# Kernel tuning notes

Hardware: AMD Instinct MI355X
Metric: run time of the kernel (lower is better)

## Reference

```python
import jax, jax.numpy as jnp
import numpy as np

P = 384   # ssm_size
H = 768   # hidden_dim
K = 4     # conv_kernel
BATCH, LEN = 16, 2048


def setup_inputs() -> dict:
    key = jax.random.key(0)
    ks = jax.random.split(key, 12)
    inputs = jax.random.normal(ks[0], (BATCH, LEN, H), jnp.float32)
    # encoder
    Wl = jax.random.normal(ks[1], (H, H), jnp.float32) / np.sqrt(H)
    bl = jnp.zeros((H,), jnp.float32)
    conv_w = jax.random.normal(ks[2], (H, 1, K), jnp.float32) / np.sqrt(K)  # depthwise
    conv_b = jnp.zeros((H,), jnp.float32)
    # selective heads (zero-init in torch; small random for a non-trivial baseline)
    Wr = jax.random.normal(ks[3], (P, H), jnp.float32) * 0.01
    Wth = jax.random.normal(ks[4], (P, H), jnp.float32) * 0.01
    Winj = jax.random.normal(ks[5], (P, H), jnp.float32) * 0.01
    # ring init: |lambda| in [0.9, 1.0], arg in (0, pi)
    u = jax.random.uniform(ks[6], (P,), jnp.float32)
    mags = jnp.sqrt(u * (1.0 ** 2 - 0.9 ** 2) + 0.9 ** 2)
    r_base = jnp.log(mags / (1.0 - mags))              # logit
    args = jax.random.uniform(ks[7], (P,), jnp.float32, minval=1e-3, maxval=np.pi - 1e-3)
    th_base = jnp.arctanh(args / np.pi)
    dt_base = jax.random.normal(ks[8], (P,), jnp.float32) * 0.5
    inj_logit = jnp.full((P,), 2.0, jnp.float32)
    b_std = 1.0 / np.sqrt(H)
    c_std = 1.0 / np.sqrt(P)
    Bp = jax.random.uniform(ks[9], (P, H, 2), jnp.float32, minval=-b_std, maxval=b_std)
    Cp = jax.random.uniform(ks[10], (H, P, 2), jnp.float32, minval=-c_std, maxval=c_std)
    D = jax.random.normal(ks[11], (H,), jnp.float32)
    return dict(inputs=inputs, Wl=Wl, bl=bl, conv_w=conv_w, conv_b=conv_b,
                Wr=Wr, Wth=Wth, Winj=Winj, r_base=r_base, th_base=th_base,
                dt_base=dt_base, inj_logit=inj_logit, Bp=Bp, Cp=Cp, D=D)


def reference(inputs, Wl, bl, conv_w, conv_b, Wr, Wth, Winj,
              r_base, th_base, dt_base, inj_logit, Bp, Cp, D):
    Bsz, L, Hd = inputs.shape
    k = conv_w.shape[-1]
    # --- encoder: linear -> silu -> causal depthwise conv -> silu ---
    feats = jax.nn.silu(inputs @ Wl.T + bl)                       # (B,L,H)
    fc = jnp.transpose(feats, (0, 2, 1))                          # (B,H,L)
    fc = jax.lax.conv_general_dilated(
        fc, conv_w, window_strides=(1,), padding=[(k - 1, 0)],
        dimension_numbers=('NCH', 'OIH', 'NCH'), feature_group_count=Hd)
    feats = jnp.transpose(jax.nn.silu(fc + conv_b[None, :, None]), (0, 2, 1))  # (B,L,H)
    # --- spectral params ---
    r = jax.nn.sigmoid(r_base + feats @ Wr.T)                     # (B,L,P)
    theta = jnp.pi * jnp.tanh(th_base + feats @ Wth.T)            # (B,L,P)
    dt_floor = 0.02
    raw_dt = jax.nn.sigmoid(dt_base)                              # (P,) per_step_dt=False
    dt = jnp.broadcast_to(dt_floor + (1.0 - dt_floor) * raw_dt, r.shape)
    r2 = jnp.maximum(r * r, 1e-8)
    dtc = jnp.maximum(dt, 1e-6)
    cos_t = jnp.cos(theta)
    # imex1 variant
    A = (r2 - 2.0 * r * cos_t + 1.0) / (dtc * dtc * r2)
    G = (1.0 - r2) / (dtc * r2)
    # --- input projection (complex) + selective injection gate ---
    Bc = Bp[..., 0] + 1j * Bp[..., 1]                             # (P,H) complex64
    Cc = Cp[..., 0] + 1j * Cp[..., 1]                             # (H,P)
    bu = inputs.astype(jnp.complex64) @ Bc.T                      # (B,L,P)
    gate = jax.nn.sigmoid(inj_logit + feats @ Winj.T)
    bu = bu * gate
    # --- D-LinOSS IMEX1 scan over time ---
    A_s = jnp.transpose(A, (1, 0, 2))                             # (L,B,P)
    G_s = jnp.transpose(G, (1, 0, 2))
    dt_s = jnp.transpose(dtc, (1, 0, 2))
    bu_s = jnp.transpose(bu, (1, 0, 2))
    z0 = jnp.zeros((Bsz, A.shape[-1]), jnp.complex64)

    def step(carry, t):
        z, x = carry
        At, Gt, dtt, but = t
        S = 1.0 / (1.0 + dtt * Gt)          # implicit damping factor
        z = S * (z - (dtt * At) * x) + (S * dtt) * but
        x = x + dtt * z
        return (z, x), x

    _, xs = jax.lax.scan(step, (z0, z0), (A_s, G_s, dt_s, bu_s))  # (L,B,P)
    states = jnp.transpose(xs, (1, 0, 2))                         # (B,L,P)
    proj = jnp.real(states @ Cc.T)                                # (B,L,H)
    return proj + inputs * D
```

## Files before the change

kernel.cpp:

```cpp
#include <hip/hip_runtime.h>
#include <math.h>

#define PP 384
#define HH 768
#define KK 4
#define BB 16
#define LL 2048
#define MM (BB*LL)
#define NCH (BB*PP)
#define NC 32
#define CLEN (LL/NC)
#define CRUN 32

typedef __attribute__((ext_vector_type(8))) short bf16x8;
typedef __attribute__((ext_vector_type(4))) float f32x4;

__device__ __forceinline__ float sigmoid_fast(float x) { return 1.0f / (1.0f + __expf(-x)); }

__device__ __forceinline__ float bf2f(unsigned short h) {
    return __uint_as_float(((unsigned int)h) << 16);
}
__device__ __forceinline__ unsigned short f2bf(float x) {
    unsigned int u = __float_as_uint(x);
    u += 0x7fff + ((u >> 16) & 1);
    return (unsigned short)(u >> 16);
}
__device__ __forceinline__ void split_bf(float x, unsigned short& hi, unsigned short& lo) {
    hi = f2bf(x);
    lo = f2bf(x - bf2f(hi));
}

__device__ __forceinline__ void gll16(const void* g, void* l) {
    __builtin_amdgcn_global_load_lds(
        (const __attribute__((address_space(1))) void*)g,
        (__attribute__((address_space(3))) void*)l, 16, 0, 0);
}

__device__ __forceinline__ void xcd_swizzle(int& bx, int& by) {
    const int gx = (int)gridDim.x;
    const int nwg = gx * (int)gridDim.y;
    const int orig = by * gx + bx;
    const int q = nwg >> 3, r = nwg & 7;
    const int xcd = orig & 7, off = orig >> 3;
    const int swz = (xcd < r ? xcd * (q + 1) : r * (q + 1) + (xcd - r) * q) + off;
    bx = swz % gx;
    by = swz / gx;
}

__device__ __forceinline__ void step_coef(float Rp, float Tp, float Ip,
    float rb, float tb, float il, float dt,
    float& c0, float& c1, float& gdt)
{
    const float PIf = 3.14159265358979323846f;
    float r  = sigmoid_fast(rb + Rp);
    float t  = tb + Tp;
    float e2 = __expf(2.0f * fabsf(t));
    float th = PIf * copysignf(1.0f - 2.0f / (e2 + 1.0f), t);
    float ct = __cosf(th);
    float r2 = fmaxf(r * r, 1e-8f);
    float Ac = (r2 - 2.0f * r * ct + 1.0f) / (dt * dt * r2);
    float Gc = (1.0f - r2) / (dt * r2);
    float S  = 1.0f / (1.0f + dt * Gc);
    float gate = sigmoid_fast(il + Ip);
    c0 = S;
    c1 = S * (dt * Ac);
    gdt = S * dt * gate;
}

__global__ __launch_bounds__(256) void repack_kernel(
    const float* __restrict__ Wl, const float* __restrict__ Wr,
    const float* __restrict__ Wth, const float* __restrict__ Winj,
    const float* __restrict__ Bp, const float* __restrict__ Cp,
    unsigned short* __restrict__ wlh, unsigned short* __restrict__ wll,
    unsigned short* __restrict__ wrth_h, unsigned short* __restrict__ wrth_l,
    unsigned short* __restrict__ winj,
    unsigned short* __restrict__ wb, unsigned short* __restrict__ wc)
{
    int i = blockIdx.x * 256 + threadIdx.x;
    const int NB = 768 * 768, NI = 384 * 768;
    if (i < NB) { split_bf(Wl[i], wlh[i], wll[i]); return; }
    i -= NB;
    if (i < NB) {
        int n = i / 768, k = i - n * 768;
        int p = n >> 1;
        float v = (n & 1) ? Wth[p * 768 + k] : Wr[p * 768 + k];
        split_bf(v, wrth_h[i], wrth_l[i]);
        return;
    }
    i -= NB;
    if (i < NI) { winj[i] = f2bf(Winj[i]); return; }
    i -= NI;
    if (i < NB) {
        int n = i / 768, k = i - n * 768;
        wb[i] = f2bf(Bp[(size_t)(n >> 1) * 1536 + k * 2 + (n & 1)]);
        return;
    }
    i -= NB;
    if (i < NB) {
        wc[i] = f2bf((i & 1) ? -Cp[i] : Cp[i]);
    }
}

__global__ __launch_bounds__(256) void split_convert_kernel(
    const float* __restrict__ in, unsigned short* __restrict__ outh,
    unsigned short* __restrict__ outl, int n4)
{
    int i = blockIdx.x * 256 + threadIdx.x;
    if (i >= n4) return;
    float4 a = ((const float4*)in)[i];
    ushort4 h, l;
    split_bf(a.x, h.x, l.x); split_bf(a.y, h.y, l.y);
    split_bf(a.z, h.z, l.z); split_bf(a.w, h.w, l.w);
    ((ushort4*)outh)[i] = h;
    ((ushort4*)outl)[i] = l;
}

template <int SMODE>
__global__ __launch_bounds__(256) void mfma_gemm_split(
    const unsigned short* __restrict__ Ah, const unsigned short* __restrict__ Al,
    const unsigned short* __restrict__ Wh, const unsigned short* __restrict__ Wl,
    float* __restrict__ Cout, int N, const float* __restrict__ bias)
{
    constexpr int K = 768;
    __shared__ unsigned short lsAh[128 * 32];
    __shared__ unsigned short lsAl[128 * 32];
    __shared__ unsigned short lsBh[128 * 32];
    __shared__ unsigned short lsBl[128 * 32];
    const int tid  = threadIdx.x;
    const int wave = tid >> 6, lane = tid & 63;
    const int wm = wave >> 1, wn = wave & 1;
    int bx = blockIdx.x, by = blockIdx.y;
    xcd_swizzle(bx, by);
    const int row0 = by * 128, col0 = bx * 128;

    const int srow = (wave << 4) + (lane >> 2);
    const int scol = (lane & 3) << 3;
    const size_t ga0 = (size_t)(row0 + srow) * K + scol;
    const size_t ga1 = (size_t)(row0 + 64 + srow) * K + scol;
    const size_t gb0 = (size_t)(col0 + srow) * K + scol;
    const size_t gb1 = (size_t)(col0 + 64 + srow) * K + scol;
    const int l0 = srow * 32 + scol;
    const int l1 = (64 + srow) * 32 + scol;

    f32x4 acc[4][4];
#pragma unroll
    for (int i = 0; i < 4; ++i)
#pragma unroll
        for (int j = 0; j < 4; ++j) acc[i][j] = (f32x4){0.f, 0.f, 0.f, 0.f};

    const int rfo = ((lane & 15) * 32) + ((lane >> 4) << 3);

    for (int kt = 0; kt < K; kt += 32) {
        __syncthreads();
        gll16(Ah + ga0 + kt, &lsAh[l0]);
        gll16(Ah + ga1 + kt, &lsAh[l1]);
        gll16(Al + ga0 + kt, &lsAl[l0]);
        gll16(Al + ga1 + kt, &lsAl[l1]);
        gll16(Wh + gb0 + kt, &lsBh[l0]);
        gll16(Wh + gb1 + kt, &lsBh[l1]);
        gll16(Wl + gb0 + kt, &lsBl[l0]);
        gll16(Wl + gb1 + kt, &lsBl[l1]);
        __syncthreads();
        bf16x8 afh[4], afl[4], bfh[4], bfl[4];
#pragma unroll
        for (int i = 0; i < 4; ++i) {
            afh[i] = *(const bf16x8*)&lsAh[(wm * 64 + i * 16) * 32 + rfo];
            afl[i] = *(const bf16x8*)&lsAl[(wm * 64 + i * 16) * 32 + rfo];
        }
#pragma unroll
        for (int j = 0; j < 4; ++j) {
            bfh[j] = *(const bf16x8*)&lsBh[(wn * 64 + j * 16) * 32 + rfo];
            bfl[j] = *(const bf16x8*)&lsBl[(wn * 64 + j * 16) * 32 + rfo];
        }
#pragma unroll
        for (int i = 0; i < 4; ++i)
#pragma unroll
            for (int j = 0; j < 4; ++j) {
                acc[i][j] = __builtin_amdgcn_mfma_f32_16x16x32_bf16(afh[i], bfh[j], acc[i][j], 0, 0, 0);
                acc[i][j] = __builtin_amdgcn_mfma_f32_16x16x32_bf16(afh[i], bfl[j], acc[i][j], 0, 0, 0);
                acc[i][j] = __builtin_amdgcn_mfma_f32_16x16x32_bf16(afl[i], bfh[j], acc[i][j], 0, 0, 0);
            }
    }

    const int rbase = row0 + wm * 64 + ((lane >> 4) << 2);
    const int cbase = col0 + wn * 64 + (lane & 15);
#pragma unroll
    for (int i = 0; i < 4; ++i) {
#pragma unroll
        for (int j = 0; j < 4; ++j) {
            const int cg = cbase + j * 16;
            float bv = (SMODE == 1) ? bias[cg] : 0.f;
#pragma unroll
            for (int q = 0; q < 4; ++q) {
                const int rg = rbase + i * 16 + q;
                const size_t off = (size_t)rg * N + cg;
                float v = acc[i][j][q];
                if (SMODE == 1) {
                    float x = v + bv;
                    Cout[off] = x * sigmoid_fast(x);
                } else {
                    Cout[off] = v;
                }
            }
        }
    }
}

template <int MODE>
__global__ __launch_bounds__(256) void mfma_gemm(
    const unsigned short* __restrict__ A, const unsigned short* __restrict__ W,
    void* __restrict__ Cout, int N,
    const unsigned short* __restrict__ resid, const float* __restrict__ Dv)
{
    constexpr int K = 768;
    __shared__ unsigned short lsA[128 * 32];
    __shared__ unsigned short lsB[128 * 32];
    const int tid  = threadIdx.x;
    const int wave = tid >> 6, lane = tid & 63;
    const int wm = wave >> 1, wn = wave & 1;
    int bx = blockIdx.x, by = blockIdx.y;
    xcd_swizzle(bx, by);
    const int row0 = by * 128, col0 = bx * 128;

    const int srow = (wave << 4) + (lane >> 2);
    const int scol = (lane & 3) << 3;
    const size_t ga0 = (size_t)(row0 + srow) * K + scol;
    const size_t ga1 = (size_t)(row0 + 64 + srow) * K + scol;
    const size_t gb0 = (size_t)(col0 + srow) * K + scol;
    const size_t gb1 = (size_t)(col0 + 64 + srow) * K + scol;
    const int l0 = srow * 32 + scol;
    const int l1 = (64 + srow) * 32 + scol;

    f32x4 acc[4][4];
#pragma unroll
    for (int i = 0; i < 4; ++i)
#pragma unroll
        for (int j = 0; j < 4; ++j) acc[i][j] = (f32x4){0.f, 0.f, 0.f, 0.f};

    const int rfo = ((lane & 15) * 32) + ((lane >> 4) << 3);

    for (int kt = 0; kt < K; kt += 32) {
        __syncthreads();
        gll16(A + ga0 + kt, &lsA[l0]);
        gll16(A + ga1 + kt, &lsA[l1]);
        gll16(W + gb0 + kt, &lsB[l0]);
        gll16(W + gb1 + kt, &lsB[l1]);
        __syncthreads();
        bf16x8 af[4], bfg[4];
#pragma unroll
        for (int i = 0; i < 4; ++i)
            af[i] = *(const bf16x8*)&lsA[(wm * 64 + i * 16) * 32 + rfo];
#pragma unroll
        for (int j = 0; j < 4; ++j)
            bfg[j] = *(const bf16x8*)&lsB[(wn * 64 + j * 16) * 32 + rfo];
#pragma unroll
        for (int i = 0; i < 4; ++i)
#pragma unroll
            for (int j = 0; j < 4; ++j)
                acc[i][j] = __builtin_amdgcn_mfma_f32_16x16x32_bf16(af[i], bfg[j], acc[i][j], 0, 0, 0);
    }

    const int rbase = row0 + wm * 64 + ((lane >> 4) << 2);
    const int cbase = col0 + wn * 64 + (lane & 15);
#pragma unroll
    for (int i = 0; i < 4; ++i) {
#pragma unroll
        for (int j = 0; j < 4; ++j) {
            const int cg = cbase + j * 16;
            const float dv = (MODE == 2) ? Dv[cg] : 0.f;
#pragma unroll
            for (int q = 0; q < 4; ++q) {
                const int rg = rbase + i * 16 + q;
                const size_t off = (size_t)rg * N + cg;
                float v = acc[i][j][q];
                if (MODE == 2) {
                    ((float*)Cout)[off] = v + bf2f(resid[off]) * dv;
                } else {
                    ((unsigned short*)Cout)[off] = f2bf(v);
                }
            }
        }
    }
}

__global__ __launch_bounds__(256) void conv_silu_kernel(
    const float* __restrict__ x, const float* __restrict__ w,
    const float* __restrict__ cb, unsigned short* __restrict__ yh,
    unsigned short* __restrict__ yl)
{
    const int NRUN = MM / CRUN;
    int tid = blockIdx.x * 256 + threadIdx.x;
    if (tid >= HH * NRUN) return;
    const int h   = tid % HH;
    const int run = tid / HH;
    const int ml0 = run * CRUN;
    const int l0  = ml0 % LL;
    const float w0 = w[h * KK + 0], w1 = w[h * KK + 1];
    const float w2 = w[h * KK + 2], w3 = w[h * KK + 3];
    const float bias = cb[h];
    float x0, x1, x2;
    if (l0 == 0) {
        x0 = 0.f; x1 = 0.f; x2 = 0.f;
    } else {
        x0 = x[(size_t)(ml0 - 3) * HH + h];
        x1 = x[(size_t)(ml0 - 2) * HH + h];
        x2 = x[(size_t)(ml0 - 1) * HH + h];
    }
    for (int i = 0; i < CRUN; ++i) {
        const size_t m = (size_t)(ml0 + i);
        const float x3 = x[m * HH + h];
        float acc = bias;
        acc = fmaf(x0, w0, acc);
        acc = fmaf(x1, w1, acc);
        acc = fmaf(x2, w2, acc);
        acc = fmaf(x3, w3, acc);
        const float y = acc * sigmoid_fast(acc);
        unsigned short hi, lo;
        split_bf(y, hi, lo);
        yh[m * HH + h] = hi;
        yl[m * HH + h] = lo;
        x0 = x1; x1 = x2; x2 = x3;
    }
}

__global__ __launch_bounds__(256) void scan_chunk_kernel(
    const float* __restrict__ heads_rt, const unsigned short* __restrict__ heads_inj,
    const unsigned short* __restrict__ bu,
    const float* __restrict__ r_base, const float* __restrict__ th_base,
    const float* __restrict__ dt_base, const float* __restrict__ inj,
    float4* __restrict__ summA, float4* __restrict__ summB)
{
    int g = blockIdx.x * 256 + threadIdx.x;
    if (g >= NC * NCH) return;
    int t = g % NCH;
    int j = g / NCH;
    int b = t / PP, p = t - b * PP;
    const float rb = r_base[p], tb = th_base[p], il = inj[p];
    const float dt = 0.02f + 0.98f * sigmoid_fast(dt_base[p]);
    float m00 = 1.f, m01 = 0.f, m10 = 0.f, m11 = 1.f;
    float vzR = 0.f, vxR = 0.f, vzI = 0.f, vxI = 0.f;
    const int mbase = b * LL + j * CLEN;
    for (int l = 0; l < CLEN; ++l) {
        const size_t m = (size_t)(mbase + l);
        const float2 rt = *(const float2*)(heads_rt + m * 768 + 2 * p);
        const float Ip = bf2f(heads_inj[m * 384 + p]);
        const ushort2 bv = *(const ushort2*)(bu + m * 768 + 2 * p);
        const float b0 = bf2f(bv.x), b1 = bf2f(bv.y);
        float c0, c1, gdt;
        step_coef(rt.x, rt.y, Ip, rb, tb, il, dt, c0, c1, gdt);
        const float azR = gdt * b0, azI = gdt * b1;
        float nm00 = c0 * m00 - c1 * m10;
        float nm01 = c0 * m01 - c1 * m11;
        m10 = fmaf(dt, nm00, m10);
        m11 = fmaf(dt, nm01, m11);
        m00 = nm00; m01 = nm01;
        float nvzR = c0 * vzR - c1 * vxR + azR;
        vxR = fmaf(dt, nvzR, vxR); vzR = nvzR;
        float nvzI = c0 * vzI - c1 * vxI + azI;
        vxI = fmaf(dt, nvzI, vxI); vzI = nvzI;
    }
    summA[g] = make_float4(m00, m01, m10, m11);
    summB[g] = make_float4(vzR, vxR, vzI, vxI);
}

__global__ __launch_bounds__(256) void scan_mid_kernel(
    const float4* __restrict__ summA, const float4* __restrict__ summB,
    float4* __restrict__ starts)
{
    int t = blockIdx.x * 256 + threadIdx.x;
    if (t >= NCH) return;
    float zR = 0.f, xR = 0.f, zI = 0.f, xI = 0.f;
    for (int j = 0; j < NC; ++j) {
        starts[j * NCH + t] = make_float4(zR, xR, zI, xI);
        float4 Mv = summA[j * NCH + t];
        float4 Vv = summB[j * NCH + t];
        float nzR = Mv.x * zR + Mv.y * xR + Vv.x;
        float nxR = Mv.z * zR + Mv.w * xR + Vv.y;
        float nzI = Mv.x * zI + Mv.y * xI + Vv.z;
        float nxI = Mv.z * zI + Mv.w * xI + Vv.w;
        zR = nzR; xR = nxR; zI = nzI; xI = nxI;
    }
}

__global__ __launch_bounds__(256) void scan_apply_kernel(
    const float* __restrict__ heads_rt, const unsigned short* __restrict__ heads_inj,
    const unsigned short* __restrict__ bu,
    const float* __restrict__ r_base, const float* __restrict__ th_base,
    const float* __restrict__ dt_base, const float* __restrict__ inj,
    const float4* __restrict__ starts, unsigned short* __restrict__ states)
{
    int g = blockIdx.x * 256 + threadIdx.x;
    if (g >= NC * NCH) return;
    int t = g % NCH;
    int j = g / NCH;
    int b = t / PP, p = t - b * PP;
    const float rb = r_base[p], tb = th_base[p], il = inj[p];
    const float dt = 0.02f + 0.98f * sigmoid_fast(dt_base[p]);
    float4 s0 = starts[j * NCH + t];
    float zR = s0.x, xR = s0.y, zI = s0.z, xI = s0.w;
    const int mbase = b * LL + j * CLEN;
    for (int l = 0; l < CLEN; ++l) {
        const size_t m = (size_t)(mbase + l);
        const float2 rt = *(const float2*)(heads_rt + m * 768 + 2 * p);
        const float Ip = bf2f(heads_inj[m * 384 + p]);
        const ushort2 bv = *(const ushort2*)(bu + m * 768 + 2 * p);
        const float b0 = bf2f(bv.x), b1 = bf2f(bv.y);
        float c0, c1, gdt;
        step_coef(rt.x, rt.y, Ip, rb, tb, il, dt, c0, c1, gdt);
        zR = c0 * zR - c1 * xR + gdt * b0;
        xR = fmaf(dt, zR, xR);
        zI = c0 * zI - c1 * xI + gdt * b1;
        xI = fmaf(dt, zI, xI);
        ushort2 sv;
        sv.x = f2bf(xR);
        sv.y = f2bf(xI);
        *(ushort2*)(states + m * 768 + 2 * p) = sv;
    }
}

extern "C" void kernel_launch(void* const* d_in, const int* in_sizes, int n_in,
                              void* d_out, int out_size, void* d_ws, size_t ws_size,
                              hipStream_t stream)
{
    const float* inputs  = (const float*)d_in[0];
    const float* Wl      = (const float*)d_in[1];
    const float* bl      = (const float*)d_in[2];
    const float* conv_w  = (const float*)d_in[3];
    const float* conv_b  = (const float*)d_in[4];
    const float* Wr      = (const float*)d_in[5];
    const float* Wth     = (const float*)d_in[6];
    const float* Winj    = (const float*)d_in[7];
    const float* r_base  = (const float*)d_in[8];
    const float* th_base = (const float*)d_in[9];
    const float* dt_base = (const float*)d_in[10];
    const float* inj_l   = (const float*)d_in[11];
    const float* Bp      = (const float*)d_in[12];
    const float* Cp      = (const float*)d_in[13];
    const float* Dv      = (const float*)d_in[14];
    float* out = (float*)d_out;

    const size_t NB = 768 * 768, NI = 384 * 768, NMH = (size_t)MM * 768;
    unsigned short* wlh    = (unsigned short*)d_ws;
    unsigned short* wll    = wlh + NB;
    unsigned short* wrth_h = wll + NB;
    unsigned short* wrth_l = wrth_h + NB;
    unsigned short* winj   = wrth_l + NB;
    unsigned short* wb     = winj + NI;
    unsigned short* wc     = wb + NB;
    unsigned short* inh    = wc + NB;
    unsigned short* inl    = inh + NMH;
    unsigned short* f2h    = inl + NMH;
    unsigned short* f2l    = f2h + NMH;
    unsigned short* hinj   = f2l + NMH;
    float* f1       = (float*)(hinj + (size_t)MM * 384);
    float* heads_rt = f1;
    float4* summA = (float4*)(f1 + NMH);
    float4* summB = summA + (size_t)NC * NCH;
    float4* starts= summB + (size_t)NC * NCH;
    unsigned short* bu = (unsigned short*)d_out;
    unsigned short* states = inl;

    {
        int total = (int)(4 * NB + NI);
        repack_kernel<<<(total + 255) / 256, 256, 0, stream>>>(
            Wl, Wr, Wth, Winj, Bp, Cp, wlh, wll, wrth_h, wrth_l, winj, wb, wc);
        int n4 = (int)(NMH / 4);
        split_convert_kernel<<<(n4 + 255) / 256, 256, 0, stream>>>(inputs, inh, inl, n4);
    }
    mfma_gemm_split<1><<<dim3(6, MM / 128), 256, 0, stream>>>(
        inh, inl, wlh, wll, f1, 768, bl);
    {
        int nthr = HH * (MM / CRUN);
        conv_silu_kernel<<<(nthr + 255) / 256, 256, 0, stream>>>(f1, conv_w, conv_b, f2h, f2l);
    }
    mfma_gemm_split<0><<<dim3(6, MM / 128), 256, 0, stream>>>(
        f2h, f2l, wrth_h, wrth_l, heads_rt, 768, nullptr);
    mfma_gemm<3><<<dim3(3, MM / 128), 256, 0, stream>>>(
        f2h, winj, (void*)hinj, 384, nullptr, nullptr);
    mfma_gemm<3><<<dim3(6, MM / 128), 256, 0, stream>>>(
        inh, wb, (void*)bu, 768, nullptr, nullptr);
    scan_chunk_kernel<<<(NC * NCH) / 256, 256, 0, stream>>>(
        heads_rt, hinj, bu, r_base, th_base, dt_base, inj_l, summA, summB);
    scan_mid_kernel<<<(NCH + 255) / 256, 256, 0, stream>>>(summA, summB, starts);
    scan_apply_kernel<<<(NC * NCH) / 256, 256, 0, stream>>>(
        heads_rt, hinj, bu, r_base, th_base, dt_base, inj_l, starts, states);
    mfma_gemm<2><<<dim3(6, MM / 128), 256, 0, stream>>>(
        states, wc, (void*)out, 768, inh, Dv);
}
```

Measured before the change: 641.1 us.

## Replace scan re-run with linear correction pass using stored transfer coefficients

The chunk pass now writes zero-start local states plus the bf16 m10/m11 entries of the per-step transfer matrix. A new elementwise kernel adds the chunk-start carry contribution to those states, replacing the second sequential scan that recomputed the step coefficients. The chunk count doubles to raise parallelism in the sequential pass. In exchange it adds writes and reads of a 4-byte-per-element correction buffer, and the bf16-rounded correction terms may lose accuracy.

```diff
diff --git a/kernel.cpp b/kernel.cpp
--- a/kernel.cpp
+++ b/kernel.cpp
@@ -8,7 +8,7 @@
 #define LL 2048
 #define MM (BB*LL)
 #define NCH (BB*PP)
-#define NC 32
+#define NC 64
 #define CLEN (LL/NC)
 #define CRUN 32
 
@@ -328,6 +328,7 @@
     const unsigned short* __restrict__ bu,
     const float* __restrict__ r_base, const float* __restrict__ th_base,
     const float* __restrict__ dt_base, const float* __restrict__ inj,
+    unsigned short* __restrict__ states, unsigned int* __restrict__ corr,
     float4* __restrict__ summA, float4* __restrict__ summB)
 {
     int g = blockIdx.x * 256 + threadIdx.x;
@@ -358,6 +359,11 @@
         vxR = fmaf(dt, nvzR, vxR); vzR = nvzR;
         float nvzI = c0 * vzI - c1 * vxI + azI;
         vxI = fmaf(dt, nvzI, vxI); vzI = nvzI;
+        ushort2 sv;
+        sv.x = f2bf(vxR);
+        sv.y = f2bf(vxI);
+        *(ushort2*)(states + m * 768 + 2 * p) = sv;
+        corr[m * 384 + p] = ((unsigned int)f2bf(m11) << 16) | (unsigned int)f2bf(m10);
     }
     summA[g] = make_float4(m00, m01, m10, m11);
     summB[g] = make_float4(vzR, vxR, vzI, vxI);
@@ -382,40 +388,34 @@
     }
 }
 
-__global__ __launch_bounds__(256) void scan_apply_kernel(
-    const float* __restrict__ heads_rt, const unsigned short* __restrict__ heads_inj,
-    const unsigned short* __restrict__ bu,
-    const float* __restrict__ r_base, const float* __restrict__ th_base,
-    const float* __restrict__ dt_base, const float* __restrict__ inj,
-    const float4* __restrict__ starts, unsigned short* __restrict__ states)
-{
-    int g = blockIdx.x * 256 + threadIdx.x;
-    if (g >= NC * NCH) return;
-    int t = g % NCH;
-    int j = g / NCH;
-    int b = t / PP, p = t - b * PP;
-    const float rb = r_base[p], tb = th_base[p], il = inj[p];
-    const float dt = 0.02f + 0.98f * sigmoid_fast(dt_base[p]);
-    float4 s0 = starts[j * NCH + t];
-    float zR = s0.x, xR = s0.y, zI = s0.z, xI = s0.w;
-    const int mbase = b * LL + j * CLEN;
-    for (int l = 0; l < CLEN; ++l) {
-        const size_t m = (size_t)(mbase + l);
-        const float2 rt = *(const float2*)(heads_rt + m * 768 + 2 * p);
-        const float Ip = bf2f(heads_inj[m * 384 + p]);
-        const ushort2 bv = *(const ushort2*)(bu + m * 768 + 2 * p);
-        const float b0 = bf2f(bv.x), b1 = bf2f(bv.y);
-        float c0, c1, gdt;
-        step_coef(rt.x, rt.y, Ip, rb, tb, il, dt, c0, c1, gdt);
-        zR = c0 * zR - c1 * xR + gdt * b0;
-        xR = fmaf(dt, zR, xR);
-        zI = c0 * zI - c1 * xI + gdt * b1;
-        xI = fmaf(dt, zI, xI);
-        ushort2 sv;
-        sv.x = f2bf(xR);
-        sv.y = f2bf(xI);
-        *(ushort2*)(states + m * 768 + 2 * p) = sv;
-    }
+__global__ __launch_bounds__(256) void scan_corr_kernel(
+    const float4* __restrict__ starts, const unsigned int* __restrict__ corr,
+    unsigned short* __restrict__ states)
+{
+    const int PH = PP / 2;
+    int i = blockIdx.x * 256 + threadIdx.x;
+    if (i >= MM * PH) return;
+    const int ph = i % PH;
+    const int m  = i / PH;
+    const int b  = m / LL;
+    const int j  = (m % LL) / CLEN;
+    const int p0 = ph * 2;
+    const int t0 = b * PP + p0;
+    float4 s0 = starts[(size_t)j * NCH + t0];
+    float4 s1 = starts[(size_t)j * NCH + t0 + 1];
+    uint2 cw = *(const uint2*)(corr + (size_t)m * 384 + p0);
+    const float a10 = bf2f((unsigned short)(cw.x & 0xffff));
+    const float a11 = bf2f((unsigned short)(cw.x >> 16));
+    const float b10 = bf2f((unsigned short)(cw.y & 0xffff));
+    const float b11 = bf2f((unsigned short)(cw.y >> 16));
+    ushort4 sv = *(ushort4*)(states + (size_t)m * 768 + 2 * p0);
+    float xR0 = bf2f(sv.x) + a10 * s0.x + a11 * s0.y;
+    float xI0 = bf2f(sv.y) + a10 * s0.z + a11 * s0.w;
+    float xR1 = bf2f(sv.z) + b10 * s1.x + b11 * s1.y;
+    float xI1 = bf2f(sv.w) + b10 * s1.z + b11 * s1.w;
+    sv.x = f2bf(xR0); sv.y = f2bf(xI0);
+    sv.z = f2bf(xR1); sv.w = f2bf(xI1);
+    *(ushort4*)(states + (size_t)m * 768 + 2 * p0) = sv;
 }
 
 extern "C" void kernel_launch(void* const* d_in, const int* in_sizes, int n_in,
@@ -459,6 +459,7 @@
     float4* starts= summB + (size_t)NC * NCH;
     unsigned short* bu = (unsigned short*)d_out;
     unsigned short* states = inl;
+    unsigned int* corr = (unsigned int*)f2h;
 
     {
         int total = (int)(4 * NB + NI);
@@ -480,10 +481,13 @@
     mfma_gemm<3><<<dim3(6, MM / 128), 256, 0, stream>>>(
         inh, wb, (void*)bu, 768, nullptr, nullptr);
     scan_chunk_kernel<<<(NC * NCH) / 256, 256, 0, stream>>>(
-        heads_rt, hinj, bu, r_base, th_base, dt_base, inj_l, summA, summB);
+        heads_rt, hinj, bu, r_base, th_base, dt_base, inj_l,
+        states, corr, summA, summB);
     scan_mid_kernel<<<(NCH + 255) / 256, 256, 0, stream>>>(summA, summB, starts);
-    scan_apply_kernel<<<(NC * NCH) / 256, 256, 0, stream>>>(
-        heads_rt, hinj, bu, r_base, th_base, dt_base, inj_l, starts, states);
+    {
+        int nthr = MM * (PP / 2);
+        scan_corr_kernel<<<(nthr + 255) / 256, 256, 0, stream>>>(starts, corr, states);
+    }
     mfma_gemm<2><<<dim3(6, MM / 128), 256, 0, stream>>>(
         states, wc, (void*)out, 768, inh, Dv);
 }
```

New measurement: 615.4 us, median of 2. 1.04x faster.
